# Performance work log

Hardware: AMD Instinct MI355X
Metric: run time of the kernel (lower is better)

The kernel has to match this reference:

```python
import jax, jax.numpy as jnp
import numpy as np

D_MODEL = 1024
NUM_HEADS = 16
D_K = D_MODEL // NUM_HEADS
ROPE_THETA = 10000.0


def setup_inputs() -> dict:
    key = jax.random.key(0)
    kx, kq, kk, kv, ko = jax.random.split(key, 5)
    B, S = 2, 2048
    sigma = np.sqrt(2.0) / np.sqrt(D_MODEL + D_MODEL)
    x = jax.random.normal(kx, (B, S, D_MODEL), dtype=jnp.float32)
    Wq = jax.random.normal(kq, (D_MODEL, D_MODEL), dtype=jnp.float32) * sigma
    Wk = jax.random.normal(kk, (D_MODEL, D_MODEL), dtype=jnp.float32) * sigma
    Wv = jax.random.normal(kv, (D_MODEL, D_MODEL), dtype=jnp.float32) * sigma
    Wo = jax.random.normal(ko, (D_MODEL, D_MODEL), dtype=jnp.float32) * sigma
    return {"x": x, "Wq": Wq, "Wk": Wk, "Wv": Wv, "Wo": Wo}


def _rope(t, positions):
    # t: [B, H, S, D_K], positions: [S]
    half = jnp.arange(0, D_K, 2, dtype=jnp.float32)          # [D_K/2]
    freqs = 1.0 / (ROPE_THETA ** (half / D_K))               # [D_K/2]
    angles = positions[:, None].astype(jnp.float32) * freqs  # [S, D_K/2]
    cos = jnp.cos(angles)
    sin = jnp.sin(angles)
    t_even = t[..., 0::2]
    t_odd = t[..., 1::2]
    even_rot = t_even * cos - t_odd * sin
    odd_rot = t_even * sin + t_odd * cos
    # interleave back to [..., D_K]
    return jnp.stack([even_rot, odd_rot], axis=-1).reshape(t.shape)


def reference(x, Wq, Wk, Wv, Wo):
    B, S, _ = x.shape
    # weight layout is [d_out, d_in]: y = x @ W.T
    def proj(W):
        y = jnp.einsum('bsd,ed->bse', x, W)
        return y.reshape(B, S, NUM_HEADS, D_K).transpose(0, 2, 1, 3)  # [B,H,S,Dk]
    Q, K, V = proj(Wq), proj(Wk), proj(Wv)
    positions = jnp.arange(S)
    Q = _rope(Q, positions)
    K = _rope(K, positions)
    scale = 1.0 / jnp.sqrt(jnp.asarray(D_K, dtype=x.dtype))
    scores = jnp.einsum('bhqd,bhkd->bhqk', Q, K) * scale  # [B,H,S,S]
    causal = jnp.tril(jnp.ones((S, S), dtype=bool))
    scores = jnp.where(causal, scores, -jnp.inf)
    probs = jax.nn.softmax(scores, axis=-1)
    out = jnp.einsum('bhqk,bhkd->bhqd', probs, V)          # [B,H,S,Dk]
    out = out.transpose(0, 2, 1, 3).reshape(B, S, D_MODEL)
    return jnp.einsum('bsd,ed->bse', out, Wo)
```

## Files before the change

kernel.cpp:

```cpp
#include <hip/hip_runtime.h>
#include <hip/hip_bf16.h>
#include <math.h>

#define S_LEN   2048
#define BATCH   2
#define DMODEL  1024
#define NHEADS  16
#define DKH     64
#define MROWS   (BATCH * S_LEN)

typedef __attribute__((ext_vector_type(8))) __bf16 bf16x8;
typedef __attribute__((ext_vector_type(4))) float f32x4;
typedef __attribute__((ext_vector_type(8))) unsigned short u16x8;

__device__ __forceinline__ float bfu2f(unsigned short u) {
    union { unsigned int i; float f; } v;
    v.i = ((unsigned int)u) << 16;
    return v.f;
}

__device__ __forceinline__ unsigned short f2bfu(float f) {
    union { __bf16 h; unsigned short u; } v;
    v.h = (__bf16)f;
    return v.u;
}

#define LGKM0() __builtin_amdgcn_s_waitcnt(0xc07f)

__device__ __forceinline__ void gload_lds16(const void* g, void* l) {
    __builtin_amdgcn_global_load_lds(
        (const __attribute__((address_space(1))) void*)g,
        (__attribute__((address_space(3))) void*)l, 16, 0, 0);
}

__global__ __launch_bounds__(256) void cvt_all(
    const float* __restrict__ W0, const float* __restrict__ W1, const float* __restrict__ W2,
    const float* __restrict__ X,
    unsigned short* __restrict__ Wb,
    unsigned short* __restrict__ Xb)
{
    const int y = blockIdx.y;
    const float* src;
    unsigned short* dst;
    if (y < 3) {
        src = (y == 0) ? W0 : (y == 1) ? W1 : W2;
        dst = Wb + (size_t)y * (DMODEL * DMODEL);
    } else {
        src = X + (size_t)(y - 3) * (DMODEL * DMODEL);
        dst = Xb + (size_t)(y - 3) * (DMODEL * DMODEL);
    }
    size_t idx = ((size_t)blockIdx.x * 256 + threadIdx.x) * 8;
    float4 a = *(const float4*)(src + idx);
    float4 b = *(const float4*)(src + idx + 4);
    u16x8 h;
    h[0] = f2bfu(a.x); h[1] = f2bfu(a.y); h[2] = f2bfu(a.z); h[3] = f2bfu(a.w);
    h[4] = f2bfu(b.x); h[5] = f2bfu(b.y); h[6] = f2bfu(b.z); h[7] = f2bfu(b.w);
    *(u16x8*)(dst + idx) = h;
}

__global__ __launch_bounds__(256) void cvt_wo(
    const float* __restrict__ W, unsigned short* __restrict__ Wob)
{
    size_t idx = ((size_t)blockIdx.x * 256 + threadIdx.x) * 8;
    float4 a = *(const float4*)(W + idx);
    float4 b = *(const float4*)(W + idx + 4);
    u16x8 h;
    h[0] = f2bfu(a.x); h[1] = f2bfu(a.y); h[2] = f2bfu(a.z); h[3] = f2bfu(a.w);
    h[4] = f2bfu(b.x); h[5] = f2bfu(b.y); h[6] = f2bfu(b.z); h[7] = f2bfu(b.w);
    *(u16x8*)(Wob + idx) = h;
}

__global__ __launch_bounds__(256) void gemm_qkv(
    const unsigned short* __restrict__ Xb,
    const unsigned short* __restrict__ Wb,
    unsigned short* __restrict__ Yq, unsigned short* __restrict__ Yk, unsigned short* __restrict__ Yv)
{
    __shared__ __align__(16) unsigned char pool[36864];
    unsigned short* As = (unsigned short*)pool;
    unsigned short* Bs = As + 128 * 32;

    const int tid  = threadIdx.x;
    const int wave = tid >> 6;
    const int lane = tid & 63;
    const int c    = lane & 15;
    const int quad = lane >> 4;

    const int m0 = blockIdx.y * 128;
    const int n0 = blockIdx.x * 128;
    const int w_idx = n0 >> 10;
    const int e0    = n0 & 1023;
    const unsigned short* Wsrc = Wb + (size_t)w_idx * (DMODEL * DMODEL);

    const int mhalf = (wave & 1) * 64;
    const int nhalf = (wave >> 1) * 64;

    f32x4 acc[4][4];
#pragma unroll
    for (int i = 0; i < 4; i++)
#pragma unroll
        for (int j = 0; j < 4; j++) acc[i][j] = (f32x4){0.f, 0.f, 0.f, 0.f};

    const int srow = wave * 32 + (lane >> 2);
    const int scol = (lane & 3) * 8;
    const unsigned short* Asrc = Xb   + (size_t)(m0 + srow) * DMODEL + scol;
    const unsigned short* Bsrc = Wsrc + (size_t)(e0 + srow) * DMODEL + scol;
    unsigned short* Adst = As + srow * 32 + scol;
    unsigned short* Bdst = Bs + srow * 32 + scol;

    for (int k0 = 0; k0 < DMODEL; k0 += 32) {
        __syncthreads();
#pragma unroll
        for (int j = 0; j < 2; j++) {
            gload_lds16(Asrc + (size_t)(j * 16) * DMODEL + k0, Adst + j * 16 * 32);
            gload_lds16(Bsrc + (size_t)(j * 16) * DMODEL + k0, Bdst + j * 16 * 32);
        }
        __syncthreads();

        bf16x8 af[4], bfr[4];
#pragma unroll
        for (int mt = 0; mt < 4; mt++)
            af[mt] = *(const bf16x8*)(&As[(mhalf + mt * 16 + c) * 32 + quad * 8]);
#pragma unroll
        for (int nt = 0; nt < 4; nt++)
            bfr[nt] = *(const bf16x8*)(&Bs[(nhalf + nt * 16 + c) * 32 + quad * 8]);
#pragma unroll
        for (int mt = 0; mt < 4; mt++)
#pragma unroll
            for (int nt = 0; nt < 4; nt++)
                acc[mt][nt] = __builtin_amdgcn_mfma_f32_16x16x32_bf16(af[mt], bfr[nt], acc[mt][nt], 0, 0, 0);
    }

    __syncthreads();

    const int h = (e0 + nhalf) >> 6;
    if (w_idx < 2) {
        unsigned short* Yqk = (w_idx == 0) ? Yq : Yk;
        float* EPf = (float*)pool + wave * 16 * 68;
        const int row = lane >> 2;
        const int cg  = lane & 3;
#pragma unroll
        for (int mt = 0; mt < 4; mt++) {
            LGKM0();
#pragma unroll
            for (int nt = 0; nt < 4; nt++)
#pragma unroll
                for (int r = 0; r < 4; r++)
                    EPf[(quad * 4 + r) * 68 + nt * 16 + c] = acc[mt][nt][r];
            LGKM0();
            float fl[16];
#pragma unroll
            for (int j = 0; j < 4; j++) {
                float4 v = *(const float4*)(&EPf[row * 68 + cg * 16 + j * 4]);
                fl[j * 4 + 0] = v.x; fl[j * 4 + 1] = v.y;
                fl[j * 4 + 2] = v.z; fl[j * 4 + 3] = v.w;
            }
            int m = m0 + mhalf + mt * 16 + row;
            int s = m & (S_LEN - 1);
            int b = m >> 11;
            u16x8 o0, o1;
#pragma unroll
            for (int pi = 0; pi < 8; pi++) {
                int p = cg * 8 + pi;
                float freq  = exp2f(-(float)p * 0.41524101186092034f);
                float angle = (float)s * freq;
                float sn, cs;
                __sincosf(angle, &sn, &cs);
                float ev = fl[2 * pi], ov = fl[2 * pi + 1];
                float re = ev * cs - ov * sn;
                float ro = ev * sn + ov * cs;
                if (pi < 4) { o0[2 * pi] = f2bfu(re); o0[2 * pi + 1] = f2bfu(ro); }
                else        { o1[2 * (pi - 4)] = f2bfu(re); o1[2 * (pi - 4) + 1] = f2bfu(ro); }
            }
            unsigned short* dst = Yqk + (((size_t)(b * NHEADS + h)) * S_LEN + s) * DKH + cg * 16;
            *(u16x8*)(dst)     = o0;
            *(u16x8*)(dst + 8) = o1;
        }
    } else {
        unsigned short* EPb = (unsigned short*)pool + wave * 64 * 72;
        LGKM0();
#pragma unroll
        for (int nt = 0; nt < 4; nt++)
#pragma unroll
            for (int mt = 0; mt < 4; mt++)
#pragma unroll
                for (int r = 0; r < 4; r++)
                    EPb[(nt * 16 + c) * 72 + mt * 16 + quad * 4 + r] = f2bfu(acc[mt][nt][r]);
        LGKM0();
        int mbase = m0 + mhalf;
        int s0 = mbase & (S_LEN - 1);
        int b  = mbase >> 11;
        unsigned short* dst = Yv + (((size_t)(b * NHEADS + h)) * DKH + lane) * S_LEN + s0;
#pragma unroll
        for (int j = 0; j < 8; j++)
            *(u16x8*)(dst + j * 8) = *(const u16x8*)(&EPb[lane * 72 + j * 8]);
    }
}

__global__ __launch_bounds__(256) void gemm_wo(
    const unsigned short* __restrict__ X,
    const unsigned short* __restrict__ Wob,
    float* __restrict__ Yf)
{
    __shared__ __align__(16) unsigned char pool[18432];
    unsigned short* As = (unsigned short*)pool;
    unsigned short* Bs = As + 64 * 32;

    const int tid  = threadIdx.x;
    const int wave = tid >> 6;
    const int lane = tid & 63;
    const int c    = lane & 15;
    const int quad = lane >> 4;

    const int m0 = blockIdx.y * 64;
    const int n0 = blockIdx.x * 128;

    const int mhalf = (wave & 1) * 32;
    const int nhalf = (wave >> 1) * 64;

    f32x4 acc[2][4];
#pragma unroll
    for (int i = 0; i < 2; i++)
#pragma unroll
        for (int j = 0; j < 4; j++) acc[i][j] = (f32x4){0.f, 0.f, 0.f, 0.f};

    const int arow = wave * 16 + (lane >> 2);
    const int brow = wave * 32 + (lane >> 2);
    const int scol = (lane & 3) * 8;
    const unsigned short* Asrc = X   + (size_t)(m0 + arow) * DMODEL + scol;
    const unsigned short* Bsrc = Wob + (size_t)(n0 + brow) * DMODEL + scol;
    unsigned short* Adst = As + arow * 32 + scol;
    unsigned short* Bdst = Bs + brow * 32 + scol;

    for (int k0 = 0; k0 < DMODEL; k0 += 32) {
        __syncthreads();
        gload_lds16(Asrc + k0, Adst);
#pragma unroll
        for (int j = 0; j < 2; j++)
            gload_lds16(Bsrc + (size_t)(j * 16) * DMODEL + k0, Bdst + j * 16 * 32);
        __syncthreads();

        bf16x8 af[2], bfr[4];
#pragma unroll
        for (int mt = 0; mt < 2; mt++)
            af[mt] = *(const bf16x8*)(&As[(mhalf + mt * 16 + c) * 32 + quad * 8]);
#pragma unroll
        for (int nt = 0; nt < 4; nt++)
            bfr[nt] = *(const bf16x8*)(&Bs[(nhalf + nt * 16 + c) * 32 + quad * 8]);
#pragma unroll
        for (int mt = 0; mt < 2; mt++)
#pragma unroll
            for (int nt = 0; nt < 4; nt++)
                acc[mt][nt] = __builtin_amdgcn_mfma_f32_16x16x32_bf16(af[mt], bfr[nt], acc[mt][nt], 0, 0, 0);
    }

    __syncthreads();

    float* EPf = (float*)pool + wave * 16 * 68;
    const int row = lane >> 2;
    const int cg  = lane & 3;
#pragma unroll
    for (int mt = 0; mt < 2; mt++) {
        LGKM0();
#pragma unroll
        for (int nt = 0; nt < 4; nt++)
#pragma unroll
            for (int r = 0; r < 4; r++)
                EPf[(quad * 4 + r) * 68 + nt * 16 + c] = acc[mt][nt][r];
        LGKM0();
        int m = m0 + mhalf + mt * 16 + row;
        float* dst = Yf + (size_t)m * DMODEL + n0 + nhalf + cg * 16;
#pragma unroll
        for (int j = 0; j < 4; j++)
            *(float4*)(dst + j * 4) = *(const float4*)(&EPf[row * 68 + cg * 16 + j * 4]);
    }
}

__global__ __launch_bounds__(256, 4) void attn_mfma(
    const unsigned short* __restrict__ Q,
    const unsigned short* __restrict__ K,
    const unsigned short* __restrict__ Vt,
    unsigned short* __restrict__ A)
{
    __shared__ unsigned short Ks[32 * 72];
    __shared__ unsigned short Vs[64 * 40];
    __shared__ unsigned short Plds[4][16 * 40];

    const int tid  = threadIdx.x;
    const int wave = tid >> 6;
    const int lane = tid & 63;
    const int c    = lane & 15;
    const int quad = lane >> 4;

    const int bh = blockIdx.x;
    const int b  = bh >> 4;
    const int h  = bh & 15;
    const int qb = (int)(gridDim.y - 1) - (int)blockIdx.y;
    const int q0b = qb * 64;
    const int q0 = q0b + wave * 16;

    const unsigned short* Qb = Q  + (size_t)bh * S_LEN * DKH;
    const unsigned short* Kb = K  + (size_t)bh * S_LEN * DKH;
    const unsigned short* Vb = Vt + (size_t)bh * DKH * S_LEN;

    bf16x8 qf0 = *(const bf16x8*)(Qb + (q0 + c) * DKH + quad * 8);
    bf16x8 qf1 = *(const bf16x8*)(Qb + (q0 + c) * DKH + 32 + quad * 8);

    f32x4 o0 = {0.f,0.f,0.f,0.f}, o1 = o0, o2 = o0, o3 = o0;
    float l[4] = {0.f, 0.f, 0.f, 0.f};

    unsigned short* Pw = &Plds[wave][0];

    const int my_nkb   = (q0 + 16 + 31) >> 5;
    const int nkb_blk  = (q0b + 64 + 31) >> 5;
    const int kb_full  = (q0 >= 31) ? (((q0 - 31) >> 5) + 1) : 0;

    const int krow  = tid >> 3;
    const int kcol8 = (tid & 7) * 8;
    const int vrow  = tid >> 2;
    const int vcol8 = (tid & 3) * 8;

    uint4 gK = *(const uint4*)(Kb + (size_t)krow * DKH + kcol8);
    uint4 gV = *(const uint4*)(Vb + (size_t)vrow * S_LEN + vcol8);

    for (int kb = 0; kb < nkb_blk; kb++) {
        const int k0 = kb * 32;
        __syncthreads();
        *(uint4*)(&Ks[krow * 72 + kcol8]) = gK;
        *(uint4*)(&Vs[vrow * 40 + vcol8]) = gV;
        __syncthreads();
        if (kb + 1 < nkb_blk) {
            gK = *(const uint4*)(Kb + (size_t)(k0 + 32 + krow) * DKH + kcol8);
            gV = *(const uint4*)(Vb + (size_t)vrow * S_LEN + k0 + 32 + vcol8);
        }
        if (kb < my_nkb) {
            bf16x8 k00 = *(const bf16x8*)(&Ks[c * 72 + quad * 8]);
            bf16x8 k01 = *(const bf16x8*)(&Ks[c * 72 + 32 + quad * 8]);
            bf16x8 k10 = *(const bf16x8*)(&Ks[(16 + c) * 72 + quad * 8]);
            bf16x8 k11 = *(const bf16x8*)(&Ks[(16 + c) * 72 + 32 + quad * 8]);
            f32x4 s0 = {0.f,0.f,0.f,0.f}, s1 = {0.f,0.f,0.f,0.f};
            s0 = __builtin_amdgcn_mfma_f32_16x16x32_bf16(qf0, k00, s0, 0, 0, 0);
            s0 = __builtin_amdgcn_mfma_f32_16x16x32_bf16(qf1, k01, s0, 0, 0, 0);
            s1 = __builtin_amdgcn_mfma_f32_16x16x32_bf16(qf0, k10, s1, 0, 0, 0);
            s1 = __builtin_amdgcn_mfma_f32_16x16x32_bf16(qf1, k11, s1, 0, 0, 0);

            if (kb < kb_full) {
#pragma unroll
                for (int r = 0; r < 4; r++) {
                    float e0 = __expf(s0[r] * 0.125f);
                    float e1 = __expf(s1[r] * 0.125f);
                    unsigned short pb0 = f2bfu(e0);
                    unsigned short pb1 = f2bfu(e1);
                    Pw[(quad * 4 + r) * 40 + c]      = pb0;
                    Pw[(quad * 4 + r) * 40 + 16 + c] = pb1;
                    l[r] += bfu2f(pb0) + bfu2f(pb1);
                }
            } else {
#pragma unroll
                for (int r = 0; r < 4; r++) {
                    int qrow = q0 + quad * 4 + r;
                    float e0 = (k0 + c      <= qrow) ? __expf(s0[r] * 0.125f) : 0.0f;
                    float e1 = (k0 + 16 + c <= qrow) ? __expf(s1[r] * 0.125f) : 0.0f;
                    unsigned short pb0 = f2bfu(e0);
                    unsigned short pb1 = f2bfu(e1);
                    Pw[(quad * 4 + r) * 40 + c]      = pb0;
                    Pw[(quad * 4 + r) * 40 + 16 + c] = pb1;
                    l[r] += bfu2f(pb0) + bfu2f(pb1);
                }
            }
            LGKM0();

            bf16x8 pf = *(const bf16x8*)(Pw + c * 40 + quad * 8);

            bf16x8 vf0 = *(const bf16x8*)(&Vs[(0 * 16 + c) * 40 + quad * 8]);
            bf16x8 vf1 = *(const bf16x8*)(&Vs[(1 * 16 + c) * 40 + quad * 8]);
            bf16x8 vf2 = *(const bf16x8*)(&Vs[(2 * 16 + c) * 40 + quad * 8]);
            bf16x8 vf3 = *(const bf16x8*)(&Vs[(3 * 16 + c) * 40 + quad * 8]);
            o0 = __builtin_amdgcn_mfma_f32_16x16x32_bf16(pf, vf0, o0, 0, 0, 0);
            o1 = __builtin_amdgcn_mfma_f32_16x16x32_bf16(pf, vf1, o1, 0, 0, 0);
            o2 = __builtin_amdgcn_mfma_f32_16x16x32_bf16(pf, vf2, o2, 0, 0, 0);
            o3 = __builtin_amdgcn_mfma_f32_16x16x32_bf16(pf, vf3, o3, 0, 0, 0);
        }
    }

#pragma unroll
    for (int m = 1; m < 16; m <<= 1) {
#pragma unroll
        for (int r = 0; r < 4; r++) l[r] += __shfl_xor(l[r], m, 64);
    }

#pragma unroll
    for (int r = 0; r < 4; r++) {
        float inv = 1.0f / l[r];
        int s = q0 + quad * 4 + r;
        unsigned short* Ap = A + ((size_t)b * S_LEN + s) * DMODEL + h * DKH;
        Ap[0 * 16 + c] = f2bfu(o0[r] * inv);
        Ap[1 * 16 + c] = f2bfu(o1[r] * inv);
        Ap[2 * 16 + c] = f2bfu(o2[r] * inv);
        Ap[3 * 16 + c] = f2bfu(o3[r] * inv);
    }
}

extern "C" void kernel_launch(void* const* d_in, const int* in_sizes, int n_in,
                              void* d_out, int out_size, void* d_ws, size_t ws_size,
                              hipStream_t stream) {
    const float* x  = (const float*)d_in[0];
    const float* Wq = (const float*)d_in[1];
    const float* Wk = (const float*)d_in[2];
    const float* Wv = (const float*)d_in[3];
    const float* Wo = (const float*)d_in[4];
    float* out = (float*)d_out;

    unsigned short* Qw = (unsigned short*)d_ws;
    unsigned short* Kw = Qw + (size_t)MROWS * DMODEL;
    unsigned short* Vw = Kw + (size_t)MROWS * DMODEL;
    unsigned short* Wb = Vw + (size_t)MROWS * DMODEL;
    unsigned short* Aw = Wb;
    unsigned short* Wob = Qw;
    unsigned short* Xb = (unsigned short*)d_out;

    cvt_all<<<dim3(DMODEL * DMODEL / (256 * 8), 7), 256, 0, stream>>>(Wq, Wk, Wv, x, Wb, Xb);

    gemm_qkv<<<dim3(3 * DMODEL / 128, MROWS / 128), 256, 0, stream>>>(
        Xb, Wb, Qw, Kw, Vw);

    attn_mfma<<<dim3(NHEADS * BATCH, S_LEN / 64), 256, 0, stream>>>(Qw, Kw, Vw, Aw);

    cvt_wo<<<dim3(DMODEL * DMODEL / (256 * 8)), 256, 0, stream>>>(Wo, Wob);

    gemm_wo<<<dim3(DMODEL / 128, MROWS / 64), 256, 0, stream>>>(Aw, Wob, out);
}
```

Baseline: 207.0 us.

## Double-buffer LDS tiles in QKV and output-projection GEMMs

Both projection GEMMs now use two LDS buffers and issue the global-to-LDS loads for the next K slice before running the MFMAs on the current one. This drops one of the two barriers per K step and lets load latency overlap compute. In exchange the Wo kernel's LDS grows from 18 KB to 24 KB, which may reduce occupancy. Correctness depends on the async LDS loads having completed by the time the barrier is reached.

```diff
diff --git a/kernel.cpp b/kernel.cpp
--- a/kernel.cpp
+++ b/kernel.cpp
@@ -76,8 +76,7 @@
     unsigned short* __restrict__ Yq, unsigned short* __restrict__ Yk, unsigned short* __restrict__ Yv)
 {
     __shared__ __align__(16) unsigned char pool[36864];
-    unsigned short* As = (unsigned short*)pool;
-    unsigned short* Bs = As + 128 * 32;
+    unsigned short* base = (unsigned short*)pool;
 
     const int tid  = threadIdx.x;
     const int wave = tid >> 6;
@@ -104,31 +103,49 @@
     const int scol = (lane & 3) * 8;
     const unsigned short* Asrc = Xb   + (size_t)(m0 + srow) * DMODEL + scol;
     const unsigned short* Bsrc = Wsrc + (size_t)(e0 + srow) * DMODEL + scol;
-    unsigned short* Adst = As + srow * 32 + scol;
-    unsigned short* Bdst = Bs + srow * 32 + scol;
-
-    for (int k0 = 0; k0 < DMODEL; k0 += 32) {
-        __syncthreads();
-#pragma unroll
-        for (int j = 0; j < 2; j++) {
-            gload_lds16(Asrc + (size_t)(j * 16) * DMODEL + k0, Adst + j * 16 * 32);
-            gload_lds16(Bsrc + (size_t)(j * 16) * DMODEL + k0, Bdst + j * 16 * 32);
-        }
-        __syncthreads();
-
-        bf16x8 af[4], bfr[4];
-#pragma unroll
-        for (int mt = 0; mt < 4; mt++)
-            af[mt] = *(const bf16x8*)(&As[(mhalf + mt * 16 + c) * 32 + quad * 8]);
-#pragma unroll
-        for (int nt = 0; nt < 4; nt++)
-            bfr[nt] = *(const bf16x8*)(&Bs[(nhalf + nt * 16 + c) * 32 + quad * 8]);
-#pragma unroll
-        for (int mt = 0; mt < 4; mt++)
-#pragma unroll
-            for (int nt = 0; nt < 4; nt++)
-                acc[mt][nt] = __builtin_amdgcn_mfma_f32_16x16x32_bf16(af[mt], bfr[nt], acc[mt][nt], 0, 0, 0);
-    }
+    const int doff = srow * 32 + scol;
+
+#define QKV_STAGE(buf, k0) do {                                                    \
+    unsigned short* _A = base + (buf) * 8192;                                      \
+    unsigned short* _B = _A + 4096;                                                \
+    _Pragma("unroll")                                                              \
+    for (int _j = 0; _j < 2; _j++) {                                               \
+        gload_lds16(Asrc + (size_t)(_j * 16) * DMODEL + (k0), _A + doff + _j * 512);\
+        gload_lds16(Bsrc + (size_t)(_j * 16) * DMODEL + (k0), _B + doff + _j * 512);\
+    }                                                                              \
+} while (0)
+
+#define QKV_COMPUTE(buf) do {                                                      \
+    const unsigned short* _A = base + (buf) * 8192;                                \
+    const unsigned short* _B = _A + 4096;                                          \
+    bf16x8 af[4], bfr[4];                                                          \
+    _Pragma("unroll")                                                              \
+    for (int mt = 0; mt < 4; mt++)                                                 \
+        af[mt] = *(const bf16x8*)(&_A[(mhalf + mt * 16 + c) * 32 + quad * 8]);     \
+    _Pragma("unroll")                                                              \
+    for (int nt = 0; nt < 4; nt++)                                                 \
+        bfr[nt] = *(const bf16x8*)(&_B[(nhalf + nt * 16 + c) * 32 + quad * 8]);    \
+    _Pragma("unroll")                                                              \
+    for (int mt = 0; mt < 4; mt++)                                                 \
+        _Pragma("unroll")                                                          \
+        for (int nt = 0; nt < 4; nt++)                                             \
+            acc[mt][nt] = __builtin_amdgcn_mfma_f32_16x16x32_bf16(af[mt], bfr[nt], acc[mt][nt], 0, 0, 0); \
+} while (0)
+
+    QKV_STAGE(0, 0);
+    __syncthreads();
+    for (int k0 = 0; k0 < DMODEL - 64; k0 += 64) {
+        QKV_STAGE(1, k0 + 32);
+        QKV_COMPUTE(0);
+        __syncthreads();
+        QKV_STAGE(0, k0 + 64);
+        QKV_COMPUTE(1);
+        __syncthreads();
+    }
+    QKV_STAGE(1, DMODEL - 32);
+    QKV_COMPUTE(0);
+    __syncthreads();
+    QKV_COMPUTE(1);
 
     __syncthreads();
 
@@ -194,6 +211,8 @@
         for (int j = 0; j < 8; j++)
             *(u16x8*)(dst + j * 8) = *(const u16x8*)(&EPb[lane * 72 + j * 8]);
     }
+#undef QKV_STAGE
+#undef QKV_COMPUTE
 }
 
 __global__ __launch_bounds__(256) void gemm_wo(
@@ -201,9 +220,8 @@
     const unsigned short* __restrict__ Wob,
     float* __restrict__ Yf)
 {
-    __shared__ __align__(16) unsigned char pool[18432];
-    unsigned short* As = (unsigned short*)pool;
-    unsigned short* Bs = As + 64 * 32;
+    __shared__ __align__(16) unsigned char pool[24576];
+    unsigned short* base = (unsigned short*)pool;
 
     const int tid  = threadIdx.x;
     const int wave = tid >> 6;
@@ -228,30 +246,49 @@
     const int scol = (lane & 3) * 8;
     const unsigned short* Asrc = X   + (size_t)(m0 + arow) * DMODEL + scol;
     const unsigned short* Bsrc = Wob + (size_t)(n0 + brow) * DMODEL + scol;
-    unsigned short* Adst = As + arow * 32 + scol;
-    unsigned short* Bdst = Bs + brow * 32 + scol;
-
-    for (int k0 = 0; k0 < DMODEL; k0 += 32) {
-        __syncthreads();
-        gload_lds16(Asrc + k0, Adst);
-#pragma unroll
-        for (int j = 0; j < 2; j++)
-            gload_lds16(Bsrc + (size_t)(j * 16) * DMODEL + k0, Bdst + j * 16 * 32);
-        __syncthreads();
-
-        bf16x8 af[2], bfr[4];
-#pragma unroll
-        for (int mt = 0; mt < 2; mt++)
-            af[mt] = *(const bf16x8*)(&As[(mhalf + mt * 16 + c) * 32 + quad * 8]);
-#pragma unroll
-        for (int nt = 0; nt < 4; nt++)
-            bfr[nt] = *(const bf16x8*)(&Bs[(nhalf + nt * 16 + c) * 32 + quad * 8]);
-#pragma unroll
-        for (int mt = 0; mt < 2; mt++)
-#pragma unroll
-            for (int nt = 0; nt < 4; nt++)
-                acc[mt][nt] = __builtin_amdgcn_mfma_f32_16x16x32_bf16(af[mt], bfr[nt], acc[mt][nt], 0, 0, 0);
-    }
+    const int adoff = arow * 32 + scol;
+    const int bdoff = brow * 32 + scol;
+
+#define WO_STAGE(buf, k0) do {                                                     \
+    unsigned short* _A = base + (buf) * 6144;                                      \
+    unsigned short* _B = _A + 2048;                                                \
+    gload_lds16(Asrc + (k0), _A + adoff);                                          \
+    _Pragma("unroll")                                                              \
+    for (int _j = 0; _j < 2; _j++)                                                 \
+        gload_lds16(Bsrc + (size_t)(_j * 16) * DMODEL + (k0), _B + bdoff + _j * 512);\
+} while (0)
+
+#define WO_COMPUTE(buf) do {                                                       \
+    const unsigned short* _A = base + (buf) * 6144;                                \
+    const unsigned short* _B = _A + 2048;                                          \
+    bf16x8 af[2], bfr[4];                                                          \
+    _Pragma("unroll")                                                              \
+    for (int mt = 0; mt < 2; mt++)                                                 \
+        af[mt] = *(const bf16x8*)(&_A[(mhalf + mt * 16 + c) * 32 + quad * 8]);     \
+    _Pragma("unroll")                                                              \
+    for (int nt = 0; nt < 4; nt++)                                                 \
+        bfr[nt] = *(const bf16x8*)(&_B[(nhalf + nt * 16 + c) * 32 + quad * 8]);    \
+    _Pragma("unroll")                                                              \
+    for (int mt = 0; mt < 2; mt++)                                                 \
+        _Pragma("unroll")                                                          \
+        for (int nt = 0; nt < 4; nt++)                                             \
+            acc[mt][nt] = __builtin_amdgcn_mfma_f32_16x16x32_bf16(af[mt], bfr[nt], acc[mt][nt], 0, 0, 0); \
+} while (0)
+
+    WO_STAGE(0, 0);
+    __syncthreads();
+    for (int k0 = 0; k0 < DMODEL - 64; k0 += 64) {
+        WO_STAGE(1, k0 + 32);
+        WO_COMPUTE(0);
+        __syncthreads();
+        WO_STAGE(0, k0 + 64);
+        WO_COMPUTE(1);
+        __syncthreads();
+    }
+    WO_STAGE(1, DMODEL - 32);
+    WO_COMPUTE(0);
+    __syncthreads();
+    WO_COMPUTE(1);
 
     __syncthreads();
 
@@ -273,6 +310,8 @@
         for (int j = 0; j < 4; j++)
             *(float4*)(dst + j * 4) = *(const float4*)(&EPf[row * 68 + cg * 16 + j * 4]);
     }
+#undef WO_STAGE
+#undef WO_COMPUTE
 }
 
 __global__ __launch_bounds__(256, 4) void attn_mfma(
```

Result: faster. 195.4 us (-5.6%).
